# Kernel optimization log

Measured on AMD Instinct MI355X. Metric: run time of the kernel, lower is better.

Reference implementation:

```python
import jax, jax.numpy as jnp
import numpy as np

B, T, V, L = 64, 2000, 29, 200
BLANK = V - 1          # Keras CTC uses last class as blank
NEG = -1e30            # large negative instead of -inf (grad-safe)
EPS = 1e-7             # keras.backend.epsilon()


def setup_inputs() -> dict:
    key = jax.random.key(0)
    k1, k2, k3, k4 = jax.random.split(key, 4)
    logits = jax.random.normal(k1, (B, T, V), dtype=jnp.float32)
    labels = jax.random.randint(k2, (B, L), 0, BLANK).astype(jnp.int32)
    # pre-conv spectrogram lengths in [2000, 4000] -> ctc lengths in [1000, 2000]
    input_length = jax.random.randint(k3, (B,), 2000, 4001).astype(jnp.int32)
    label_length = jax.random.randint(k4, (B,), 50, L + 1).astype(jnp.int32)
    return {"logits": logits, "labels": labels, "input_length": input_length,
            "label_length": label_length, "max_time_steps": 4000}


def _ctc_loss(log_probs, labels, ctc_len, label_len):
    """Standard CTC forward DP in log space. log_probs: [B,T,V]."""
    Bn, Tn, Vn = log_probs.shape
    Ln = labels.shape[1]
    S = 2 * Ln + 1
    # extended label sequence: blank, l1, blank, l2, ..., blank
    ext = jnp.full((Bn, S), BLANK, dtype=jnp.int32).at[:, 1::2].set(labels)
    # gather per-lattice-position log-probs: [B, T, S]
    lp_ext = jnp.take_along_axis(log_probs, ext[:, None, :], axis=2)
    s_idx = jnp.arange(S)
    ext_m2 = jnp.concatenate([jnp.full((Bn, 2), -1, jnp.int32), ext[:, :-2]], axis=1)
    skip_ok = (s_idx[None, :] >= 2) & (ext != BLANK) & (ext != ext_m2)

    alpha0 = (jnp.full((Bn, S), NEG, jnp.float32)
              .at[:, 0].set(lp_ext[:, 0, 0])
              .at[:, 1].set(lp_ext[:, 0, 1]))
    negcol = jnp.full((Bn, 1), NEG, jnp.float32)

    def step(alpha, xt):
        lp_t, t = xt
        p1 = jnp.concatenate([negcol, alpha[:, :-1]], axis=1)
        p2 = jnp.concatenate([negcol, negcol, alpha[:, :-2]], axis=1)
        p2 = jnp.where(skip_ok, p2, NEG)
        new = jnp.logaddexp(jnp.logaddexp(alpha, p1), p2) + lp_t
        alpha = jnp.where((t < ctc_len)[:, None], new, alpha)
        return alpha, None

    ts = jnp.arange(1, Tn)
    alpha, _ = jax.lax.scan(step, alpha0, (jnp.swapaxes(lp_ext, 0, 1)[1:], ts))

    i1 = (2 * label_len)[:, None]
    i2 = jnp.maximum(2 * label_len - 1, 0)[:, None]
    a1 = jnp.take_along_axis(alpha, i1, axis=1)[:, 0]
    a2 = jnp.take_along_axis(alpha, i2, axis=1)[:, 0]
    return -jnp.logaddexp(a1, a2)


def reference(logits, labels, input_length, label_length, max_time_steps):
    Tc = logits.shape[1]
    # compute_length_after_conv: floor(input_length * T_ctc / max_time_steps)
    ctc_len = jnp.floor(
        (input_length * Tc).astype(jnp.float32) / jnp.float32(max_time_steps)
    ).astype(jnp.int32)
    # ctc_batch_cost: y_pred are softmax probs, then log(y_pred + eps)
    log_probs = jnp.log(jax.nn.softmax(logits, axis=-1) + EPS)
    loss = _ctc_loss(log_probs, labels, ctc_len, label_length)
    return loss[:, None]  # [B, 1] like keras ctc_batch_cost
```

## Files before the change

### kernel.cpp

```cpp
#include <hip/hip_runtime.h>
#include <math.h>

#define Bn 64
#define Tn 2000
#define Vn 29
#define Ln 200
#define Sn 401
#define BLANKC 28
#define EPSF  1e-7f
#define CHUNK 128
#define TSTR  132
#define SENT  (-(1 << 20))
#define LN2F  0.69314718055994531f

__device__ __forceinline__ float getc(const float4& v, int u) {
    return u == 0 ? v.x : u == 1 ? v.y : u == 2 ? v.z : v.w;
}
__device__ __forceinline__ float dpp_shr1_f(float x) {
    return __int_as_float(__builtin_amdgcn_update_dpp(
        0, __float_as_int(x), 0x138, 0xF, 0xF, true));
}
__device__ __forceinline__ int dpp_shr1_i(int x) {
    return __builtin_amdgcn_update_dpp(0, x, 0x138, 0xF, 0xF, true);
}
__device__ __forceinline__ float dpp_shl1_f(float x) {
    return __int_as_float(__builtin_amdgcn_update_dpp(
        0, __float_as_int(x), 0x130, 0xF, 0xF, true));
}
__device__ __forceinline__ int dpp_shl1_i(int x) {
    return __builtin_amdgcn_update_dpp(0, x, 0x130, 0xF, 0xF, true);
}
__device__ __forceinline__ float dscale(int d) {
    return (d > 0 || d < -126) ? 0.f : __int_as_float((127 + d) << 23);
}

#define ALIGNF_                                                                  \
  const int EeF_ = zf_f ? SENT : E_f;                                            \
  const int EnF_ = max(EeF_, Enb_f);                                             \
  const float snF_ = dscale(EeF_ - EnF_), sbF_ = dscale(Enb_f - EnF_);           \
  float w[8];                                                                    \
  _Pragma("unroll") for (int k = 0; k < 8; ++k) w[k] = a_f[k] * snF_;

#define PREFF_(POUT, PC, TOFFN)                                                  \
  { const int tf_ = (TOFFN) > (CHUNK-4) ? (CHUNK-4) : (TOFFN);                   \
    _Pragma("unroll") for (int m = 0; m < 4; ++m)                                \
      POUT[m] = *(const float4*)((PC) + soffF[m] + tf_);                         \
    POUT[4] = *(const float4*)((PC) + BLANKC * TSTR + tf_); }

#define STEPF_(PIN, u) {                                                         \
    const float n7_ = dpp_shr1_f(w[7]) * sbF_;                                   \
    const float pb_ = getc(PIN[4], u);                                           \
    w[7] = (fmaf(skF[3], w[5], w[7]) + w[6]) * getc(PIN[3], u);                  \
    w[6] = (w[6] + w[5]) * pb_;                                                  \
    w[5] = (fmaf(skF[2], w[3], w[5]) + w[4]) * getc(PIN[2], u);                  \
    w[4] = (w[4] + w[3]) * pb_;                                                  \
    w[3] = (fmaf(skF[1], w[1], w[3]) + w[2]) * getc(PIN[1], u);                  \
    w[2] = (w[2] + w[1]) * pb_;                                                  \
    w[1] = (fmaf(skF[0], n7_, w[1]) + w[0]) * getc(PIN[0], u);                   \
    w[0] = (w[0] + n7_) * pb_; }

#define FINF_                                                                    \
  float mxF_ = fmaxf(fmaxf(fmaxf(w[0],w[1]),fmaxf(w[2],w[3])),                   \
                     fmaxf(fmaxf(w[4],w[5]),fmaxf(w[6],w[7])));                  \
  const bool zF_ = !(mxF_ > 0.f);                                                \
  const int eF_ = ((__float_as_int(mxF_) >> 23) & 255) - 126;                    \
  const int EnewF_ = EnF_ + eF_;                                                 \
  Enb_f = dpp_shr1_i(zF_ ? SENT : EnewF_);                                       \
  if (lane == 0) Enb_f = SENT;                                                   \
  const float rsF_ = __int_as_float((127 - eF_) << 23);                          \
  _Pragma("unroll") for (int k = 0; k < 8; ++k) a_f[k] = w[k] * rsF_;            \
  E_f = EnewF_; zf_f = zF_;

#define ROUNDF(T0, PIN, POUT, PC, TOFFN) do {                                    \
  ALIGNF_  PREFF_(POUT, PC, TOFFN)                                               \
  _Pragma("unroll") for (int u = 0; u < 4; ++u) {                                \
    const int t_ = (T0) + u;                                                     \
    if (t_ != 0 && t_ < TFe) STEPF_(PIN, u)                                      \
  }                                                                              \
  FINF_                                                                          \
} while (0)

#define ROUNDF_NG(PIN, POUT, PC, TOFFN) do {                                     \
  ALIGNF_  PREFF_(POUT, PC, TOFFN)                                               \
  STEPF_(PIN, 0) STEPF_(PIN, 1) STEPF_(PIN, 2) STEPF_(PIN, 3)                    \
  FINF_                                                                          \
} while (0)

#define ALIGNB_                                                                  \
  const int EeB_ = zf_b ? SENT : E_b;                                            \
  const int EnB_ = max(EeB_, Enb_b);                                             \
  const float snB_ = dscale(EeB_ - EnB_), sbB_ = dscale(Enb_b - EnB_);           \
  float w[8];                                                                    \
  _Pragma("unroll") for (int k = 0; k < 8; ++k) w[k] = a_b[k] * snB_;

#define PREFB_(POUT, PC, TOFFN)                                                  \
  { const int tf_ = (TOFFN) > (CHUNK-4) ? (CHUNK-4) : (TOFFN);                   \
    _Pragma("unroll") for (int m = 0; m < 4; ++m)                                \
      POUT[m] = *(const float4*)((PC) + soffB[m] + tf_);                         \
    POUT[4] = *(const float4*)((PC) + BLANKC * TSTR + tf_); }

#define STEPB_(PIN, u) {                                                         \
    const float pb_ = getc(PIN[4], u);                                           \
    const float q0_ = w[0] * pb_;                                                \
    const float q1_ = w[1] * getc(PIN[0], u);                                    \
    const float n8_ = dpp_shl1_f(q0_) * sbB_;                                    \
    const float n9_ = dpp_shl1_f(q1_) * sbB_;                                    \
    const float q2_ = w[2] * pb_;                                                \
    const float q3_ = w[3] * getc(PIN[1], u);                                    \
    const float q4_ = w[4] * pb_;                                                \
    const float q5_ = w[5] * getc(PIN[2], u);                                    \
    const float q6_ = w[6] * pb_;                                                \
    const float q7_ = w[7] * getc(PIN[3], u);                                    \
    w[0] = q0_ + q1_;                                                            \
    w[1] = fmaf(skB[0], q3_, q1_) + q2_;                                         \
    w[2] = q2_ + q3_;                                                            \
    w[3] = fmaf(skB[1], q5_, q3_) + q4_;                                         \
    w[4] = q4_ + q5_;                                                            \
    w[5] = fmaf(skB[2], q7_, q5_) + q6_;                                         \
    w[6] = q6_ + q7_;                                                            \
    w[7] = fmaf(skB[3], n9_, q7_) + n8_; }

#define FINB_                                                                    \
  float mxB_ = fmaxf(fmaxf(fmaxf(w[0],w[1]),fmaxf(w[2],w[3])),                   \
                     fmaxf(fmaxf(w[4],w[5]),fmaxf(w[6],w[7])));                  \
  const bool zB_ = !(mxB_ > 0.f);                                                \
  const int eB_ = ((__float_as_int(mxB_) >> 23) & 255) - 126;                    \
  const int EnewB_ = EnB_ + eB_;                                                 \
  Enb_b = dpp_shl1_i(zB_ ? SENT : EnewB_);                                       \
  if (lane == 63) Enb_b = SENT;                                                  \
  const float rsB_ = __int_as_float((127 - eB_) << 23);                          \
  _Pragma("unroll") for (int k = 0; k < 8; ++k) a_b[k] = w[k] * rsB_;            \
  E_b = EnewB_; zf_b = zB_;

#define ROUNDB(S0, PIN, POUT, PC, TOFFN) do {                                    \
  ALIGNB_  PREFB_(POUT, PC, TOFFN)                                               \
  _Pragma("unroll") for (int u = 0; u < 4; ++u) {                                \
    const int s_ = (S0) + u;                                                     \
    if (s_ < TBe) STEPB_(PIN, u)                                                 \
  }                                                                              \
  FINB_                                                                          \
} while (0)

#define ROUNDB_NG(PIN, POUT, PC, TOFFN) do {                                     \
  ALIGNB_  PREFB_(POUT, PC, TOFFN)                                               \
  STEPB_(PIN, 0) STEPB_(PIN, 1) STEPB_(PIN, 2) STEPB_(PIN, 3)                    \
  FINB_                                                                          \
} while (0)

__global__ __launch_bounds__(256, 1)
void ctc_live_kernel(const float* __restrict__ logits,
                     const int*   __restrict__ labels,
                     const int*   __restrict__ input_length,
                     const int*   __restrict__ label_length,
                     const int*   __restrict__ mts_ptr,
                     float*       __restrict__ out)
{
    __shared__ __align__(16) float PFb[2][Vn * TSTR];
    __shared__ __align__(16) float PBb[2][Vn * TSTR];

    const int b    = blockIdx.x;
    const int tid  = threadIdx.x;
    const int wid  = tid >> 6;
    const int lane = tid & 63;
    const float* lg  = logits + (size_t)b * Tn * Vn;
    const int*   lab = labels + b * Ln;

    const int mts = *mts_ptr;
    const int ctc_len = (int)floorf((float)(input_length[b] * Tn) / (float)mts);
    const int tend = min(max(ctc_len, 1), Tn);
    const int tm   = (tend - 1) >> 1;
    const int TFe  = tm + 1;
    const int TBe  = tend - 1 - tm;
    const int nchF = (TFe + CHUNK - 1) / CHUNK;
    const int nchB = (TBe + CHUNK - 1) / CHUNK;
    const int nch2 = max(nchF, nchB);

    int soffF[4]; float skF[4];
    #pragma unroll
    for (int m = 0; m < 4; ++m) {
        const int s = 8 * lane + 2 * m + 1;
        int e = BLANKC; float sk = 0.f;
        if (s < Sn) {
            const int li = (s - 1) >> 1;
            e = lab[li];
            if (s >= 3 && e != lab[li - 1]) sk = 1.f;
        }
        soffF[m] = e * TSTR; skF[m] = sk;
    }
    int soffB[4]; float skB[4];
    #pragma unroll
    for (int m = 0; m < 4; ++m) {
        const int s = 8 * lane + 2 * m + 1;
        soffB[m] = ((s < Sn) ? lab[(s - 1) >> 1] : BLANKC) * TSTR;
        const int ssrc = s + 2;
        float sk = 0.f;
        if (ssrc < Sn) {
            const int li = (ssrc - 1) >> 1;
            if (lab[li] != lab[li - 1]) sk = 1.f;
        }
        skB[m] = sk;
    }

    auto srow = [&](const float* row, float* Pb, int i) {
        float x[Vn]; float mm = -INFINITY;
        #pragma unroll
        for (int v = 0; v < Vn; ++v) { x[v] = row[v]; mm = fmaxf(mm, x[v]); }
        float z = 0.f;
        #pragma unroll
        for (int v = 0; v < Vn; ++v) { x[v] = __expf(x[v] - mm); z += x[v]; }
        const float rz = 1.0f / z;
        #pragma unroll
        for (int v = 0; v < Vn; ++v) Pb[v * TSTR + i] = x[v] * rz + EPSF;
    };
    auto stageF = [&](int c) {
        const int base = c * CHUNK;
        const int fill = min(CHUNK, TFe - base);
        float* Pb = PFb[c & 1];
        for (int i = lane; i < fill; i += 64)
            srow(lg + (size_t)(base + i) * Vn, Pb, i);
    };
    auto stageB = [&](int c) {
        const int base = c * CHUNK;
        const int fill = min(CHUNK, TBe - base);
        float* Pb = PBb[c & 1];
        for (int i = lane; i < fill; i += 64)
            srow(lg + (size_t)(tend - 1 - (base + i)) * Vn, Pb, i);
    };

    if (wid == 2) stageF(0);
    if (wid == 3 && TBe > 0) stageB(0);
    __syncthreads();

    float a_f[8] = {0.f,0.f,0.f,0.f,0.f,0.f,0.f,0.f};
    float a_b[8] = {0.f,0.f,0.f,0.f,0.f,0.f,0.f,0.f};
    int   E_f = 0, Enb_f = SENT, E_b = 0, Enb_b = SENT;
    bool  zf_f = true, zf_b = true;
    float4 qAf[5], qBf[5], qAb[5], qBb[5];

    if (wid == 0) {
        __builtin_amdgcn_s_setprio(1);
        if (lane == 0) {
            a_f[0] = PFb[0][BLANKC * TSTR];
            a_f[1] = PFb[0][soffF[0]];
        }
        zf_f = (lane != 0);
        Enb_f = dpp_shr1_i(zf_f ? SENT : 0);
        if (lane == 0) Enb_f = SENT;
    } else if (wid == 1) {
        __builtin_amdgcn_s_setprio(1);
        const int ll = label_length[b];
        const int s1 = 2 * ll, s2 = max(2 * ll - 1, 0);
        #pragma unroll
        for (int k = 0; k < 8; ++k) {
            const int s = 8 * lane + k;
            a_b[k] = (s == s1 || s == s2) ? 0.5f : 0.f;
        }
        E_b  = 1;
        zf_b = !(((s1 >> 3) == lane) || ((s2 >> 3) == lane));
        Enb_b = dpp_shl1_i(zf_b ? SENT : E_b);
        if (lane == 63) Enb_b = SENT;
    }

    for (int c = 0; c < nch2; ++c) {
        if (wid == 2) {
            if (c + 1 < nchF) stageF(c + 1);
        } else if (wid == 3) {
            if (c + 1 < nchB) stageB(c + 1);
        } else if (wid == 0) {
            if (c < nchF) {
                float* Pc = PFb[c & 1];
                const int rbase = c * CHUNK;
                const int rcnt  = min(CHUNK, TFe - rbase);
                const int nr    = (rcnt + 3) >> 2;
                const int nfull = min((TFe - rbase) >> 2, nr);
                #pragma unroll
                for (int m = 0; m < 4; ++m)
                    qAf[m] = *(const float4*)(Pc + soffF[m]);
                qAf[4] = *(const float4*)(Pc + BLANKC * TSTR);

                int jj = 0;
                if (c == 0) {
                    ROUNDF(0, qAf, qBf, Pc, 4);
                    ROUNDF(4, qBf, qAf, Pc, 8);
                    jj = 2;
                }
                for (; jj + 2 <= nfull; jj += 2) {
                    ROUNDF_NG(qAf, qBf, Pc, 4 * (jj + 1));
                    ROUNDF_NG(qBf, qAf, Pc, 4 * (jj + 2));
                }
                for (; jj < nr; jj += 2) {
                    ROUNDF(rbase + 4 * jj,       qAf, qBf, Pc, 4 * (jj + 1));
                    ROUNDF(rbase + 4 * (jj + 1), qBf, qAf, Pc, 4 * (jj + 2));
                }
            }
        } else {
            if (c < nchB) {
                float* Pc = PBb[c & 1];
                const int sbase = c * CHUNK;
                const int rcnt  = min(CHUNK, TBe - sbase);
                const int nr    = (rcnt + 3) >> 2;
                const int nfull = min((TBe - sbase) >> 2, nr);
                #pragma unroll
                for (int m = 0; m < 4; ++m)
                    qAb[m] = *(const float4*)(Pc + soffB[m]);
                qAb[4] = *(const float4*)(Pc + BLANKC * TSTR);

                int jj = 0;
                for (; jj + 2 <= nfull; jj += 2) {
                    ROUNDB_NG(qAb, qBb, Pc, 4 * (jj + 1));
                    ROUNDB_NG(qBb, qAb, Pc, 4 * (jj + 2));
                }
                for (; jj < nr; jj += 2) {
                    ROUNDB(sbase + 4 * jj,       qAb, qBb, Pc, 4 * (jj + 1));
                    ROUNDB(sbase + 4 * (jj + 1), qBb, qAb, Pc, 4 * (jj + 2));
                }
            }
        }
        __syncthreads();
    }

    float* AFa = PFb[0];
    int*   ELa = (int*)(PFb[0] + 512);
    float* AFb = PBb[0];
    int*   ELb = (int*)(PBb[0] + 512);

    if (wid == 0) {
        #pragma unroll
        for (int k = 0; k < 8; ++k) AFa[lane * 8 + k] = a_f[k];
        ELa[lane] = zf_f ? SENT : E_f;
    } else if (wid == 1) {
        #pragma unroll
        for (int k = 0; k < 8; ++k) AFb[lane * 8 + k] = a_b[k];
        ELb[lane] = zf_b ? SENT : E_b;
    }
    __syncthreads();

    if (wid == 0) {
        float v = 0.f;
        #pragma unroll
        for (int k = 0; k < 8; ++k)
            v = fmaf(AFa[lane * 8 + k], AFb[lane * 8 + k], v);
        const int el  = ELa[lane] + ELb[lane];
        const bool val = (v > 0.f);
        int em = val ? el : (SENT * 2);
        #pragma unroll
        for (int off = 1; off < 64; off <<= 1)
            em = max(em, __shfl_xor(em, off, 64));
        float sv = val ? ldexpf(v, el - em) : 0.f;
        #pragma unroll
        for (int off = 1; off < 64; off <<= 1)
            sv += __shfl_xor(sv, off, 64);
        if (lane == 0) out[b] = -(__logf(sv) + (float)em * LN2F);
    }
}

extern "C" void kernel_launch(void* const* d_in, const int* in_sizes, int n_in,
                              void* d_out, int out_size, void* d_ws, size_t ws_size,
                              hipStream_t stream) {
    const float* logits       = (const float*)d_in[0];
    const int*   labels       = (const int*)d_in[1];
    const int*   input_length = (const int*)d_in[2];
    const int*   label_length = (const int*)d_in[3];
    const int*   mts          = (const int*)d_in[4];
    float* out = (float*)d_out;

    ctc_live_kernel<<<Bn, 256, 0, stream>>>(logits, labels, input_length,
                                            label_length, mts, out);
}
```

Before: 81.17 us.

## Process 16 time steps per renormalization round in CTC forward/backward DP

Each DP round now covers 16 time steps instead of 4 before rescaling the alpha/beta values. It prefetches four float4 groups per lattice column from shared memory. This amortizes the per-round max/exponent renormalization, DPP exchange and LDS prefetch latency over more steps. The cost is much higher register pressure from the 4x5 float4 buffers, plus the risk of float underflow or overflow across 16 unnormalized steps.

```diff
diff --git a/kernel.cpp b/kernel.cpp
--- a/kernel.cpp
+++ b/kernel.cpp
@@ -41,11 +41,12 @@
   float w[8];                                                                    \
   _Pragma("unroll") for (int k = 0; k < 8; ++k) w[k] = a_f[k] * snF_;
 
-#define PREFF_(POUT, PC, TOFFN)                                                  \
-  { const int tf_ = (TOFFN) > (CHUNK-4) ? (CHUNK-4) : (TOFFN);                   \
-    _Pragma("unroll") for (int m = 0; m < 4; ++m)                                \
-      POUT[m] = *(const float4*)((PC) + soffF[m] + tf_);                         \
-    POUT[4] = *(const float4*)((PC) + BLANKC * TSTR + tf_); }
+#define PREFF16_(POUT, PC, TOFFN)                                                \
+  { const int tf_ = (TOFFN) > (CHUNK-16) ? (CHUNK-16) : (TOFFN);                 \
+    _Pragma("unroll") for (int q = 0; q < 4; ++q) {                              \
+      _Pragma("unroll") for (int m = 0; m < 4; ++m)                              \
+        POUT[q][m] = *(const float4*)((PC) + soffF[m] + tf_ + 4 * q);            \
+      POUT[q][4] = *(const float4*)((PC) + BLANKC * TSTR + tf_ + 4 * q); } }
 
 #define STEPF_(PIN, u) {                                                         \
     const float n7_ = dpp_shr1_f(w[7]) * sbF_;                                   \
@@ -71,18 +72,22 @@
   _Pragma("unroll") for (int k = 0; k < 8; ++k) a_f[k] = w[k] * rsF_;            \
   E_f = EnewF_; zf_f = zF_;
 
-#define ROUNDF(T0, PIN, POUT, PC, TOFFN) do {                                    \
-  ALIGNF_  PREFF_(POUT, PC, TOFFN)                                               \
-  _Pragma("unroll") for (int u = 0; u < 4; ++u) {                                \
-    const int t_ = (T0) + u;                                                     \
-    if (t_ != 0 && t_ < TFe) STEPF_(PIN, u)                                      \
-  }                                                                              \
+#define ROUNDF16(T0, PIN, POUT, PC, TOFFN) do {                                  \
+  ALIGNF_  PREFF16_(POUT, PC, TOFFN)                                             \
+  _Pragma("unroll") for (int q = 0; q < 4; ++q) {                                \
+    _Pragma("unroll") for (int u = 0; u < 4; ++u) {                              \
+      const int t_ = (T0) + 4 * q + u;                                           \
+      if (t_ != 0 && t_ < TFe) STEPF_(PIN[q], u)                                 \
+    } }                                                                          \
   FINF_                                                                          \
 } while (0)
 
-#define ROUNDF_NG(PIN, POUT, PC, TOFFN) do {                                     \
-  ALIGNF_  PREFF_(POUT, PC, TOFFN)                                               \
-  STEPF_(PIN, 0) STEPF_(PIN, 1) STEPF_(PIN, 2) STEPF_(PIN, 3)                    \
+#define ROUNDF16_NG(PIN, POUT, PC, TOFFN) do {                                   \
+  ALIGNF_  PREFF16_(POUT, PC, TOFFN)                                             \
+  STEPF_(PIN[0], 0) STEPF_(PIN[0], 1) STEPF_(PIN[0], 2) STEPF_(PIN[0], 3)        \
+  STEPF_(PIN[1], 0) STEPF_(PIN[1], 1) STEPF_(PIN[1], 2) STEPF_(PIN[1], 3)        \
+  STEPF_(PIN[2], 0) STEPF_(PIN[2], 1) STEPF_(PIN[2], 2) STEPF_(PIN[2], 3)        \
+  STEPF_(PIN[3], 0) STEPF_(PIN[3], 1) STEPF_(PIN[3], 2) STEPF_(PIN[3], 3)        \
   FINF_                                                                          \
 } while (0)
 
@@ -93,11 +98,12 @@
   float w[8];                                                                    \
   _Pragma("unroll") for (int k = 0; k < 8; ++k) w[k] = a_b[k] * snB_;
 
-#define PREFB_(POUT, PC, TOFFN)                                                  \
-  { const int tf_ = (TOFFN) > (CHUNK-4) ? (CHUNK-4) : (TOFFN);                   \
-    _Pragma("unroll") for (int m = 0; m < 4; ++m)                                \
-      POUT[m] = *(const float4*)((PC) + soffB[m] + tf_);                         \
-    POUT[4] = *(const float4*)((PC) + BLANKC * TSTR + tf_); }
+#define PREFB16_(POUT, PC, TOFFN)                                                \
+  { const int tf_ = (TOFFN) > (CHUNK-16) ? (CHUNK-16) : (TOFFN);                 \
+    _Pragma("unroll") for (int q = 0; q < 4; ++q) {                              \
+      _Pragma("unroll") for (int m = 0; m < 4; ++m)                              \
+        POUT[q][m] = *(const float4*)((PC) + soffB[m] + tf_ + 4 * q);            \
+      POUT[q][4] = *(const float4*)((PC) + BLANKC * TSTR + tf_ + 4 * q); } }
 
 #define STEPB_(PIN, u) {                                                         \
     const float pb_ = getc(PIN[4], u);                                           \
@@ -132,28 +138,32 @@
   _Pragma("unroll") for (int k = 0; k < 8; ++k) a_b[k] = w[k] * rsB_;            \
   E_b = EnewB_; zf_b = zB_;
 
-#define ROUNDB(S0, PIN, POUT, PC, TOFFN) do {                                    \
-  ALIGNB_  PREFB_(POUT, PC, TOFFN)                                               \
-  _Pragma("unroll") for (int u = 0; u < 4; ++u) {                                \
-    const int s_ = (S0) + u;                                                     \
-    if (s_ < TBe) STEPB_(PIN, u)                                                 \
-  }                                                                              \
+#define ROUNDB16(S0, PIN, POUT, PC, TOFFN) do {                                  \
+  ALIGNB_  PREFB16_(POUT, PC, TOFFN)                                             \
+  _Pragma("unroll") for (int q = 0; q < 4; ++q) {                                \
+    _Pragma("unroll") for (int u = 0; u < 4; ++u) {                              \
+      const int s_ = (S0) + 4 * q + u;                                           \
+      if (s_ < TBe) STEPB_(PIN[q], u)                                            \
+    } }                                                                          \
   FINB_                                                                          \
 } while (0)
 
-#define ROUNDB_NG(PIN, POUT, PC, TOFFN) do {                                     \
-  ALIGNB_  PREFB_(POUT, PC, TOFFN)                                               \
-  STEPB_(PIN, 0) STEPB_(PIN, 1) STEPB_(PIN, 2) STEPB_(PIN, 3)                    \
+#define ROUNDB16_NG(PIN, POUT, PC, TOFFN) do {                                   \
+  ALIGNB_  PREFB16_(POUT, PC, TOFFN)                                             \
+  STEPB_(PIN[0], 0) STEPB_(PIN[0], 1) STEPB_(PIN[0], 2) STEPB_(PIN[0], 3)        \
+  STEPB_(PIN[1], 0) STEPB_(PIN[1], 1) STEPB_(PIN[1], 2) STEPB_(PIN[1], 3)        \
+  STEPB_(PIN[2], 0) STEPB_(PIN[2], 1) STEPB_(PIN[2], 2) STEPB_(PIN[2], 3)        \
+  STEPB_(PIN[3], 0) STEPB_(PIN[3], 1) STEPB_(PIN[3], 2) STEPB_(PIN[3], 3)        \
   FINB_                                                                          \
 } while (0)
 
 __global__ __launch_bounds__(256, 1)
-void ctc_live_kernel(const float* __restrict__ logits,
-                     const int*   __restrict__ labels,
-                     const int*   __restrict__ input_length,
-                     const int*   __restrict__ label_length,
-                     const int*   __restrict__ mts_ptr,
-                     float*       __restrict__ out)
+void ctc_r16_kernel(const float* __restrict__ logits,
+                    const int*   __restrict__ labels,
+                    const int*   __restrict__ input_length,
+                    const int*   __restrict__ label_length,
+                    const int*   __restrict__ mts_ptr,
+                    float*       __restrict__ out)
 {
     __shared__ __align__(16) float PFb[2][Vn * TSTR];
     __shared__ __align__(16) float PBb[2][Vn * TSTR];
@@ -235,7 +245,7 @@
     float a_b[8] = {0.f,0.f,0.f,0.f,0.f,0.f,0.f,0.f};
     int   E_f = 0, Enb_f = SENT, E_b = 0, Enb_b = SENT;
     bool  zf_f = true, zf_b = true;
-    float4 qAf[5], qBf[5], qAb[5], qBb[5];
+    float4 qA[4][5], qB[4][5];
 
     if (wid == 0) {
         __builtin_amdgcn_s_setprio(1);
@@ -271,26 +281,29 @@
                 float* Pc = PFb[c & 1];
                 const int rbase = c * CHUNK;
                 const int rcnt  = min(CHUNK, TFe - rbase);
-                const int nr    = (rcnt + 3) >> 2;
-                const int nfull = min((TFe - rbase) >> 2, nr);
+                const int nr    = (rcnt + 15) >> 4;
+                const int nfull = min((TFe - rbase) >> 4, nr);
                 #pragma unroll
-                for (int m = 0; m < 4; ++m)
-                    qAf[m] = *(const float4*)(Pc + soffF[m]);
-                qAf[4] = *(const float4*)(Pc + BLANKC * TSTR);
+                for (int q = 0; q < 4; ++q) {
+                    #pragma unroll
+                    for (int m = 0; m < 4; ++m)
+                        qA[q][m] = *(const float4*)(Pc + soffF[m] + 4 * q);
+                    qA[q][4] = *(const float4*)(Pc + BLANKC * TSTR + 4 * q);
+                }
 
                 int jj = 0;
                 if (c == 0) {
-                    ROUNDF(0, qAf, qBf, Pc, 4);
-                    ROUNDF(4, qBf, qAf, Pc, 8);
+                    ROUNDF16(0,  qA, qB, Pc, 16);
+                    ROUNDF16(16, qB, qA, Pc, 32);
                     jj = 2;
                 }
                 for (; jj + 2 <= nfull; jj += 2) {
-                    ROUNDF_NG(qAf, qBf, Pc, 4 * (jj + 1));
-                    ROUNDF_NG(qBf, qAf, Pc, 4 * (jj + 2));
+                    ROUNDF16_NG(qA, qB, Pc, 16 * (jj + 1));
+                    ROUNDF16_NG(qB, qA, Pc, 16 * (jj + 2));
                 }
                 for (; jj < nr; jj += 2) {
-                    ROUNDF(rbase + 4 * jj,       qAf, qBf, Pc, 4 * (jj + 1));
-                    ROUNDF(rbase + 4 * (jj + 1), qBf, qAf, Pc, 4 * (jj + 2));
+                    ROUNDF16(rbase + 16 * jj,       qA, qB, Pc, 16 * (jj + 1));
+                    ROUNDF16(rbase + 16 * (jj + 1), qB, qA, Pc, 16 * (jj + 2));
                 }
             }
         } else {
@@ -298,21 +311,24 @@
                 float* Pc = PBb[c & 1];
                 const int sbase = c * CHUNK;
                 const int rcnt  = min(CHUNK, TBe - sbase);
-                const int nr    = (rcnt + 3) >> 2;
-                const int nfull = min((TBe - sbase) >> 2, nr);
+                const int nr    = (rcnt + 15) >> 4;
+                const int nfull = min((TBe - sbase) >> 4, nr);
                 #pragma unroll
-                for (int m = 0; m < 4; ++m)
-                    qAb[m] = *(const float4*)(Pc + soffB[m]);
-                qAb[4] = *(const float4*)(Pc + BLANKC * TSTR);
+                for (int q = 0; q < 4; ++q) {
+                    #pragma unroll
+                    for (int m = 0; m < 4; ++m)
+                        qA[q][m] = *(const float4*)(Pc + soffB[m] + 4 * q);
+                    qA[q][4] = *(const float4*)(Pc + BLANKC * TSTR + 4 * q);
+                }
 
                 int jj = 0;
                 for (; jj + 2 <= nfull; jj += 2) {
-                    ROUNDB_NG(qAb, qBb, Pc, 4 * (jj + 1));
-                    ROUNDB_NG(qBb, qAb, Pc, 4 * (jj + 2));
+                    ROUNDB16_NG(qA, qB, Pc, 16 * (jj + 1));
+                    ROUNDB16_NG(qB, qA, Pc, 16 * (jj + 2));
                 }
                 for (; jj < nr; jj += 2) {
-                    ROUNDB(sbase + 4 * jj,       qAb, qBb, Pc, 4 * (jj + 1));
-                    ROUNDB(sbase + 4 * (jj + 1), qBb, qAb, Pc, 4 * (jj + 2));
+                    ROUNDB16(sbase + 16 * jj,       qA, qB, Pc, 16 * (jj + 1));
+                    ROUNDB16(sbase + 16 * (jj + 1), qB, qA, Pc, 16 * (jj + 2));
                 }
             }
         }
@@ -364,6 +380,6 @@
     const int*   mts          = (const int*)d_in[4];
     float* out = (float*)d_out;
 
-    ctc_live_kernel<<<Bn, 256, 0, stream>>>(logits, labels, input_length,
-                                            label_length, mts, out);
-}
+    ctc_r16_kernel<<<Bn, 256, 0, stream>>>(logits, labels, input_length,
+                                           label_length, mts, out);
+}
```

New measurement: 67.08 us. 1.21x faster.
